# Optimization experiments

Hardware: AMD Instinct MI355X
Metric: run time of the kernel (lower is better)

## Reference

```python
import jax, jax.numpy as jnp
import numpy as np

EPS = 1e-05
H, N, F = 1024, 16, 4096  # hidden_dim, state_dim, ffn_dim


def layernorm(x, g, b):
    mu = jnp.mean(x, axis=-1, keepdims=True)
    var = jnp.mean(jnp.square(x - mu), axis=-1, keepdims=True)
    return (x - mu) * jax.lax.rsqrt(var + EPS) * g + b


def setup_inputs() -> dict:
    key = jax.random.key(0)
    ks = jax.random.split(key, 12)
    B, L = 2, 2048
    s = lambda fan_in: 1.0 / np.sqrt(fan_in)
    inp = {
        "x": jax.random.normal(ks[0], (B, L, H), jnp.float32),
        "ln1_g": jnp.ones((H,), jnp.float32),
        "ln1_b": jnp.zeros((H,), jnp.float32),
        "Wd": jax.random.uniform(ks[1], (H, H), jnp.float32, -s(H), s(H)),
        "bd": jnp.zeros((H,), jnp.float32),
        "Wbc": jax.random.uniform(ks[2], (2 * N, H), jnp.float32, -s(H), s(H)),
        "bbc": jnp.zeros((2 * N,), jnp.float32),
        "A_log": jnp.log(jnp.tile(jnp.arange(1, N + 1, dtype=jnp.float32), (H, 1))),
        "D": jnp.ones((H,), jnp.float32),
        "ln2_g": jnp.ones((H,), jnp.float32),
        "ln2_b": jnp.zeros((H,), jnp.float32),
        "W1": jax.random.uniform(ks[3], (F, H), jnp.float32, -s(H), s(H)),
        "b1": jnp.zeros((F,), jnp.float32),
        "W2": jax.random.uniform(ks[4], (H, F), jnp.float32, -s(F), s(F)),
        "b2": jnp.zeros((H,), jnp.float32),
    }
    return inp


def _selective_ssm(xn, delta, Bm, Cm, A, D):
    # xn: (B,L,H)  delta: (B,L,H)  Bm,Cm: (B,L,N)  A: (H,N)  D: (H,)
    Bsz = xn.shape[0]
    # time-major for scan
    xs = (jnp.moveaxis(delta, 1, 0), jnp.moveaxis(Bm, 1, 0),
          jnp.moveaxis(Cm, 1, 0), jnp.moveaxis(xn, 1, 0))

    def step(h, t):
        d_t, b_t, c_t, x_t = t  # (B,H), (B,N), (B,N), (B,H)
        dA = jnp.exp(d_t[:, :, None] * A)                      # (B,H,N)
        dBx = d_t[:, :, None] * b_t[:, None, :] * x_t[:, :, None]
        h = dA * h + dBx                                       # (B,H,N)
        y = jnp.einsum('bhn,bn->bh', h, c_t)                   # (B,H)
        return h, y

    h0 = jnp.zeros((Bsz, H, N), xn.dtype)
    _, ys = jax.lax.scan(step, h0, xs)
    y = jnp.moveaxis(ys, 0, 1)  # (B,L,H)
    return y + D * xn


def reference(x, ln1_g, ln1_b, Wd, bd, Wbc, bbc, A_log, D,
              ln2_g, ln2_b, W1, b1, W2, b2):
    # --- SSMLayer: pre-norm selective SSM + residual ---
    xn = layernorm(x, ln1_g, ln1_b)
    delta = jax.nn.softplus(xn @ Wd.T + bd)      # (B,L,H)
    bc = xn @ Wbc.T + bbc                        # (B,L,2N)
    Bm, Cm = bc[..., :N], bc[..., N:]
    A = -jnp.exp(A_log)                          # (H,N), negative real
    ssm_out = x + _selective_ssm(xn, delta, Bm, Cm, A, D)
    # --- MambaBlock: norm -> FFN -> residual with ssm_out ---
    normed = layernorm(ssm_out, ln2_g, ln2_b)
    hff = jax.nn.gelu(normed @ W1.T + b1, approximate=False)
    ffn_out = hff @ W2.T + b2
    return ffn_out + ssm_out
```

## Files before the change

### kernel.cpp

```cpp
#include <hip/hip_runtime.h>
#include <cstdint>
#include <cstddef>

typedef unsigned short USHORT;
typedef __bf16 bf16x8 __attribute__((ext_vector_type(8)));
typedef float f32x4 __attribute__((ext_vector_type(4)));

__device__ __forceinline__ float b2f(USHORT u) {
    union { unsigned int i; float f; } v; v.i = ((unsigned int)u) << 16; return v.f;
}
__device__ __forceinline__ USHORT f2bf(float f) {
    union { float f; unsigned int i; } v; v.f = f;
    unsigned int u = v.i;
    unsigned int r = (u + 0x7FFFu + ((u >> 16) & 1u)) >> 16;
    return (USHORT)r;
}
__device__ __forceinline__ float fexp2(float x) { return __builtin_amdgcn_exp2f(x); }

__device__ __forceinline__ void gload_lds16(const void* g, void* l) {
    __builtin_amdgcn_global_load_lds(
        (const __attribute__((address_space(1))) void*)(uintptr_t)g,
        (__attribute__((address_space(3))) void*)(uint32_t)(uintptr_t)l,
        16, 0, 0);
}

__global__ __launch_bounds__(256)
void f2b_all(const float* __restrict__ Wd, const float* __restrict__ W1,
             const float* __restrict__ W2, const float* __restrict__ Wbc,
             USHORT* __restrict__ WdB, USHORT* __restrict__ W1B,
             USHORT* __restrict__ W2B, USHORT* __restrict__ WbcB)
{
    const size_t u = (size_t)blockIdx.x * 256 + threadIdx.x;
    const float* src; USHORT* dst; size_t base;
    if (u < 262144)       { src = Wd;  dst = WdB;  base = 0; }
    else if (u < 1310720) { src = W1;  dst = W1B;  base = 262144; }
    else if (u < 2359296) { src = W2;  dst = W2B;  base = 1310720; }
    else                  { src = Wbc; dst = WbcB; base = 2359296; }
    const size_t i = (u - base) * 4;
    float4 v = *(const float4*)(src + i);
    ushort4 o;
    o.x = f2bf(v.x); o.y = f2bf(v.y); o.z = f2bf(v.z); o.w = f2bf(v.w);
    *(ushort4*)(dst + i) = o;
}

__global__ __launch_bounds__(256)
void ln_kernel(const float* __restrict__ inp, const float* __restrict__ g,
               const float* __restrict__ bsh, USHORT* __restrict__ out)
{
    const int tid = threadIdx.x;
    const int lane = tid & 63;
    const size_t row = (size_t)blockIdx.x * 4 + (tid >> 6);
    const float4* ip = (const float4*)inp + row * 256;
    float4 v[4];
    float s = 0.f, sq = 0.f;
    #pragma unroll
    for (int q = 0; q < 4; q++) {
        v[q] = ip[lane + 64 * q];
        s  += v[q].x + v[q].y + v[q].z + v[q].w;
        sq += v[q].x*v[q].x + v[q].y*v[q].y + v[q].z*v[q].z + v[q].w*v[q].w;
    }
    #pragma unroll
    for (int off = 32; off; off >>= 1) { s += __shfl_xor(s, off); sq += __shfl_xor(sq, off); }
    const float mu = s * (1.0f / 1024.0f);
    const float var = sq * (1.0f / 1024.0f) - mu * mu;
    const float rs = rsqrtf(var + 1e-5f);
    ushort4* op = (ushort4*)out + row * 256;
    #pragma unroll
    for (int q = 0; q < 4; q++) {
        float4 gv = ((const float4*)g)[lane + 64 * q];
        float4 bv = ((const float4*)bsh)[lane + 64 * q];
        ushort4 o;
        o.x = f2bf((v[q].x - mu) * rs * gv.x + bv.x);
        o.y = f2bf((v[q].y - mu) * rs * gv.y + bv.y);
        o.z = f2bf((v[q].z - mu) * rs * gv.z + bv.z);
        o.w = f2bf((v[q].w - mu) * rs * gv.w + bv.w);
        op[lane + 64 * q] = o;
    }
}

template<int EPI>
__global__ __launch_bounds__(256)
void gemm_bt(const USHORT* __restrict__ A, const USHORT* __restrict__ B,
             const float* __restrict__ bias, void* __restrict__ outp,
             void* __restrict__ outp2, int M, int N, int K, int lda, int ldb)
{
    __shared__ __align__(16) unsigned char smem[32768];
    USHORT* As = (USHORT*)smem;
    USHORT* Bs = (USHORT*)(smem + 8192);
    const int tid = threadIdx.x;
    const int lane = tid & 63;
    const int w = tid >> 6;
    const int wr = w >> 1, wc = w & 1;

    const int nx = gridDim.x, ny = gridDim.y;
    const int pid = blockIdx.y * nx + blockIdx.x;
    const int npg = 8 * nx;
    const int gid = pid / npg;
    const int first = gid * 8;
    const int rem = ny - first;
    const int gsz = (rem < 8) ? rem : 8;
    const int py = first + (pid % npg) % gsz;
    const int px = (pid % npg) / gsz;
    const int tm = py * 128;
    const int tn = px * 128;

    f32x4 acc[4][4];
    #pragma unroll
    for (int i = 0; i < 4; i++)
        #pragma unroll
        for (int j = 0; j < 4; j++) acc[i][j] = (f32x4){0.f, 0.f, 0.f, 0.f};

    const int srow = tid >> 2;
    const int scol = (tid & 3) * 8;
    const USHORT* gA0 = A + (size_t)(tm + srow) * lda + scol;
    const USHORT* gA1 = A + (size_t)(tm + 64 + srow) * lda + scol;
    const USHORT* gB0 = B + (size_t)(tn + srow) * ldb + scol;
    const USHORT* gB1 = B + (size_t)(tn + 64 + srow) * ldb + scol;
    USHORT* lA0 = As + w * 512;
    USHORT* lA1 = As + 2048 + w * 512;
    USHORT* lB0 = Bs + w * 512;
    USHORT* lB1 = Bs + 2048 + w * 512;

    const int fr = lane & 15;
    const int fko = (lane >> 4) * 8;
    const int quad = lane >> 4;

    for (int k0 = 0; k0 < K; k0 += 64) {
        gload_lds16(gA0 + k0, lA0);
        gload_lds16(gA1 + k0, lA1);
        gload_lds16(gB0 + k0, lB0);
        gload_lds16(gB1 + k0, lB1);
        gload_lds16(gA0 + k0 + 32, lA0 + 8192);
        gload_lds16(gA1 + k0 + 32, lA1 + 8192);
        gload_lds16(gB0 + k0 + 32, lB0 + 8192);
        gload_lds16(gB1 + k0 + 32, lB1 + 8192);
        __syncthreads();
        #pragma unroll
        for (int h = 0; h < 2; h++) {
            const USHORT* Ah = As + h * 8192;
            const USHORT* Bh = Bs + h * 8192;
            bf16x8 af[4], bfr[4];
            #pragma unroll
            for (int i = 0; i < 4; i++) {
                af[i]  = *(const bf16x8*)(Ah + (wr * 64 + i * 16 + fr) * 32 + fko);
                bfr[i] = *(const bf16x8*)(Bh + (wc * 64 + i * 16 + fr) * 32 + fko);
            }
            #pragma unroll
            for (int i = 0; i < 4; i++)
                #pragma unroll
                for (int j = 0; j < 4; j++)
                    acc[i][j] = __builtin_amdgcn_mfma_f32_16x16x32_bf16(af[i], bfr[j], acc[i][j], 0, 0, 0);
        }
        __syncthreads();
    }

    float* eW = (float*)(smem + (size_t)w * 4352);
    const int rr = lane >> 5;
    const int cc = lane & 31;
    const int gcolb = tn + wc * 64;
    float2 bvv = *(const float2*)&bias[gcolb + cc * 2];

    #pragma unroll
    for (int i = 0; i < 4; i++) {
        #pragma unroll
        for (int j = 0; j < 4; j++)
            #pragma unroll
            for (int r = 0; r < 4; r++)
                eW[(quad * 4 + r) * 68 + j * 16 + fr] = acc[i][j][r];
        __syncthreads();
        const int grow0 = tm + wr * 64 + i * 16;
        #pragma unroll
        for (int rp = 0; rp < 8; rp++) {
            const int row = rp * 2 + rr;
            const float2 v = *(const float2*)&eW[row * 68 + cc * 2];
            const size_t gidx = (size_t)(grow0 + row) * N + gcolb + cc * 2;
            if constexpr (EPI == 2) {
                const float z0 = v.x + bvv.x, z1 = v.y + bvv.y;
                const float o0 = (z0 > 20.f) ? z0 : 0.69314718f * __log2f(1.f + fexp2(z0 * 1.44269504f));
                const float o1 = (z1 > 20.f) ? z1 : 0.69314718f * __log2f(1.f + fexp2(z1 * 1.44269504f));
                *(float2*)((float*)outp + gidx) = make_float2(o0, o1);
            }
        }
        __syncthreads();
    }
    (void)outp2; (void)M;
}

template<int EPI>
__global__ __launch_bounds__(512)
void gemm256(const USHORT* __restrict__ A, const USHORT* __restrict__ B,
             const float* __restrict__ bias, void* __restrict__ outp,
             void* __restrict__ outp2, int M, int N, int K, int lda, int ldb)
{
    __shared__ __align__(16) unsigned char smem[131072];
    const int tid = threadIdx.x;
    const int lane = tid & 63;
    const int w = tid >> 6;
    const int wr = w >> 2;
    const int wc = w & 3;

    const int gx = gridDim.x;
    const int pid = blockIdx.y * gx + blockIdx.x;
    const int nwg = gx * gridDim.y;
    const int cpx = nwg >> 3;
    const int s = (pid & 7) * cpx + (pid >> 3);
    const int c4 = s >> 4;
    const int w4 = s & 15;
    const int py = ((c4 >> 2) << 2) + (w4 >> 2);
    const int px = ((c4 & 3) << 2) + (w4 & 3);
    const int tm = py * 256;
    const int tn = px * 256;

    USHORT* po = nullptr;
    if constexpr (EPI == 3) {
        const int z = blockIdx.z;
        A += (size_t)z * K;
        B += (size_t)z * K;
        po = ((z < 2) ? (USHORT*)outp : (USHORT*)outp2) + (size_t)(z & 1) * ((size_t)M * N);
    }

    const int sr = tid >> 2;
    const int su = (tid & 3) ^ ((tid >> 3) & 3);
    const USHORT* gA0 = A + (size_t)(tm + sr) * lda + su * 8;
    const USHORT* gA1 = A + (size_t)(tm + 128 + sr) * lda + su * 8;
    const USHORT* gB0 = B + (size_t)(tn + sr) * ldb + su * 8;
    const USHORT* gB1 = B + (size_t)(tn + 128 + sr) * ldb + su * 8;

    const int fr = lane & 15;
    const int quad = lane >> 4;
    const int uR = quad ^ ((fr >> 1) & 3);
    const int loff = fr * 32 + uR * 8;

    f32x4 acc[8][4];
    #pragma unroll
    for (int i = 0; i < 8; i++)
        #pragma unroll
        for (int j = 0; j < 4; j++) acc[i][j] = (f32x4){0.f, 0.f, 0.f, 0.f};

    const int NT = K >> 5;

    auto stage = [&](int t) {
        unsigned char* sb = smem + (size_t)(t & 3) * 32768;
        const size_t koff = (size_t)t * 32;
        gload_lds16(gA0 + koff, sb + w * 1024);
        gload_lds16(gA1 + koff, sb + 8192 + w * 1024);
        gload_lds16(gB0 + koff, sb + 16384 + w * 1024);
        gload_lds16(gB1 + koff, sb + 24576 + w * 1024);
    };

    stage(0);
    stage(1);

    for (int t = 0; t < NT; ++t) {
        if (t + 1 < NT) asm volatile("s_waitcnt vmcnt(4)" ::: "memory");
        else            asm volatile("s_waitcnt vmcnt(0)" ::: "memory");
        __builtin_amdgcn_s_barrier();
        if (t + 2 < NT) stage(t + 2);

        const USHORT* sA = (const USHORT*)(smem + (size_t)(t & 3) * 32768);
        const USHORT* sB = sA + 8192;
        bf16x8 a[4], b[4];
        #pragma unroll
        for (int j = 0; j < 4; j++)
            b[j] = *(const bf16x8*)(sB + (wc * 64 + j * 16) * 32 + loff);
        #pragma unroll
        for (int i = 0; i < 4; i++)
            a[i] = *(const bf16x8*)(sA + (wr * 128 + i * 16) * 32 + loff);
        __builtin_amdgcn_s_setprio(1);
        #pragma unroll
        for (int i = 0; i < 4; i++)
            #pragma unroll
            for (int j = 0; j < 4; j++)
                acc[i][j] = __builtin_amdgcn_mfma_f32_16x16x32_bf16(a[i], b[j], acc[i][j], 0, 0, 0);
        __builtin_amdgcn_s_setprio(0);
        #pragma unroll
        for (int i = 0; i < 4; i++)
            a[i] = *(const bf16x8*)(sA + (wr * 128 + 64 + i * 16) * 32 + loff);
        __builtin_amdgcn_s_setprio(1);
        #pragma unroll
        for (int i = 0; i < 4; i++)
            #pragma unroll
            for (int j = 0; j < 4; j++)
                acc[4 + i][j] = __builtin_amdgcn_mfma_f32_16x16x32_bf16(a[i], b[j], acc[4 + i][j], 0, 0, 0);
        __builtin_amdgcn_s_setprio(0);
    }

    float* eW = (float*)(smem + (size_t)w * 4352);
    const int erow = lane >> 2;
    const int ecq = lane & 3;
    const int gcolb = tn + wc * 64 + ecq * 16;
    float bb[16];
    if constexpr (EPI == 1) {
        #pragma unroll
        for (int q = 0; q < 4; q++) {
            float4 bv = *(const float4*)&bias[gcolb + q * 4];
            bb[q*4+0] = bv.x; bb[q*4+1] = bv.y; bb[q*4+2] = bv.z; bb[q*4+3] = bv.w;
        }
    }
    #pragma unroll
    for (int i = 0; i < 8; i++) {
        #pragma unroll
        for (int j = 0; j < 4; j++)
            #pragma unroll
            for (int r = 0; r < 4; r++)
                eW[(quad * 4 + r) * 68 + j * 16 + fr] = acc[i][j][r];
        float v[16];
        #pragma unroll
        for (int q = 0; q < 4; q++) {
            float4 t4 = *(const float4*)&eW[erow * 68 + ecq * 16 + q * 4];
            v[q*4+0] = t4.x; v[q*4+1] = t4.y; v[q*4+2] = t4.z; v[q*4+3] = t4.w;
        }
        const int grow = tm + wr * 128 + i * 16 + erow;
        uint32_t pk[8];
        if constexpr (EPI == 1) {
            #pragma unroll
            for (int q = 0; q < 8; q++) {
                const float z0 = v[2*q]   + bb[2*q];
                const float z1 = v[2*q+1] + bb[2*q+1];
                const float u0 = z0 * (0.7978845608f + 0.035677408f * z0 * z0);
                const float u1 = z1 * (0.7978845608f + 0.035677408f * z1 * z1);
                const float s0 = __builtin_amdgcn_rcpf(1.f + fexp2(2.885390082f * u0));
                const float s1 = __builtin_amdgcn_rcpf(1.f + fexp2(2.885390082f * u1));
                const float g0 = z0 * (1.f - s0), g1 = z1 * (1.f - s1);
                pk[q] = (uint32_t)f2bf(g0) | ((uint32_t)f2bf(g1) << 16);
            }
            USHORT* op = (USHORT*)outp + (size_t)grow * N + gcolb;
            *(uint4*)op = make_uint4(pk[0], pk[1], pk[2], pk[3]);
            *(uint4*)(op + 8) = make_uint4(pk[4], pk[5], pk[6], pk[7]);
        } else {
            #pragma unroll
            for (int q = 0; q < 8; q++)
                pk[q] = (uint32_t)f2bf(v[2*q]) | ((uint32_t)f2bf(v[2*q+1]) << 16);
            USHORT* op = po + (size_t)grow * N + gcolb;
            *(uint4*)op = make_uint4(pk[0], pk[1], pk[2], pk[3]);
            *(uint4*)(op + 8) = make_uint4(pk[4], pk[5], pk[6], pk[7]);
        }
    }
}

template<int EPI>
__global__ __launch_bounds__(512)
void gemm_tlp(const USHORT* __restrict__ A, const USHORT* __restrict__ B,
              const float* __restrict__ bias, void* __restrict__ outp,
              void* __restrict__ outp2, int M, int N, int K, int lda, int ldb)
{
    __shared__ __align__(16) unsigned char smem[73728];
    const int tid = threadIdx.x;
    const int lane = tid & 63;
    const int w = tid >> 6;
    const int wr = w >> 2;
    const int wc = w & 3;

    const int gx = gridDim.x;
    const int pid = blockIdx.y * gx + blockIdx.x;
    const int nwg = gx * gridDim.y;
    const int cpx = nwg >> 3;
    const int sw = (pid & 7) * cpx + (pid >> 3);
    const int tm = (sw >> 2) * 128;
    const int tn = (sw & 3) * 256;

    USHORT* po = nullptr;
    if constexpr (EPI == 3) {
        const int z = blockIdx.z;
        A += (size_t)z * K;
        B += (size_t)z * K;
        po = ((z < 2) ? (USHORT*)outp : (USHORT*)outp2) + (size_t)(z & 1) * ((size_t)M * N);
    }

    const int srow = tid >> 2;
    const int su = (tid & 3) ^ ((tid >> 3) & 3);
    const USHORT* gA  = A + (size_t)(tm + srow) * lda + su * 8;
    const USHORT* gB0 = B + (size_t)(tn + srow) * ldb + su * 8;
    const USHORT* gB1 = B + (size_t)(tn + 128 + srow) * ldb + su * 8;

    const int fr = lane & 15;
    const int quad = lane >> 4;
    const int uR = quad ^ ((fr >> 1) & 3);
    const int loff = fr * 32 + uR * 8;

    f32x4 acc[4][4];
    #pragma unroll
    for (int i = 0; i < 4; i++)
        #pragma unroll
        for (int j = 0; j < 4; j++) acc[i][j] = (f32x4){0.f, 0.f, 0.f, 0.f};

    const int NT = K >> 5;

    auto stage = [&](int t) {
        unsigned char* sb = smem + (size_t)(t % 3) * 24576;
        const size_t ko = (size_t)t * 32;
        gload_lds16(gA  + ko, sb +         w * 1024);
        gload_lds16(gB0 + ko, sb +  8192 + w * 1024);
        gload_lds16(gB1 + ko, sb + 16384 + w * 1024);
    };

    stage(0);
    stage(1);

    for (int t = 0; t < NT; ++t) {
        if (t + 2 < NT) { stage(t + 2); asm volatile("s_waitcnt vmcnt(6)" ::: "memory"); }
        else if (t + 1 < NT) asm volatile("s_waitcnt vmcnt(3)" ::: "memory");
        else                 asm volatile("s_waitcnt vmcnt(0)" ::: "memory");
        __builtin_amdgcn_s_barrier();

        const USHORT* sA = (const USHORT*)(smem + (size_t)(t % 3) * 24576);
        const USHORT* sB = sA + 4096;
        bf16x8 a[4], b[4];
        #pragma unroll
        for (int j = 0; j < 4; j++)
            b[j] = *(const bf16x8*)(sB + (wc * 64 + j * 16) * 32 + loff);
        #pragma unroll
        for (int i = 0; i < 4; i++)
            a[i] = *(const bf16x8*)(sA + (wr * 64 + i * 16) * 32 + loff);
        __builtin_amdgcn_s_setprio(1);
        #pragma unroll
        for (int i = 0; i < 4; i++)
            #pragma unroll
            for (int j = 0; j < 4; j++)
                acc[i][j] = __builtin_amdgcn_mfma_f32_16x16x32_bf16(a[i], b[j], acc[i][j], 0, 0, 0);
        __builtin_amdgcn_s_setprio(0);
        __builtin_amdgcn_s_barrier();
    }

    __syncthreads();
    float* eW = (float*)(smem + (size_t)w * 4352);
    const int erow = lane >> 2;
    const int ecq = lane & 3;
    const int gcolb = tn + wc * 64 + ecq * 16;
    float bb[16];
    if constexpr (EPI == 1) {
        #pragma unroll
        for (int q = 0; q < 4; q++) {
            float4 bv = *(const float4*)&bias[gcolb + q * 4];
            bb[q*4+0] = bv.x; bb[q*4+1] = bv.y; bb[q*4+2] = bv.z; bb[q*4+3] = bv.w;
        }
    }
    #pragma unroll
    for (int i = 0; i < 4; i++) {
        #pragma unroll
        for (int j = 0; j < 4; j++)
            #pragma unroll
            for (int r = 0; r < 4; r++)
                eW[(quad * 4 + r) * 68 + j * 16 + fr] = acc[i][j][r];
        float v[16];
        #pragma unroll
        for (int q = 0; q < 4; q++) {
            float4 t4 = *(const float4*)&eW[erow * 68 + ecq * 16 + q * 4];
            v[q*4+0] = t4.x; v[q*4+1] = t4.y; v[q*4+2] = t4.z; v[q*4+3] = t4.w;
        }
        const int grow = tm + wr * 64 + i * 16 + erow;
        uint32_t pk[8];
        if constexpr (EPI == 1) {
            #pragma unroll
            for (int q = 0; q < 8; q++) {
                const float z0 = v[2*q]   + bb[2*q];
                const float z1 = v[2*q+1] + bb[2*q+1];
                const float u0 = z0 * (0.7978845608f + 0.035677408f * z0 * z0);
                const float u1 = z1 * (0.7978845608f + 0.035677408f * z1 * z1);
                const float s0 = __builtin_amdgcn_rcpf(1.f + fexp2(2.885390082f * u0));
                const float s1 = __builtin_amdgcn_rcpf(1.f + fexp2(2.885390082f * u1));
                const float g0 = z0 * (1.f - s0), g1 = z1 * (1.f - s1);
                pk[q] = (uint32_t)f2bf(g0) | ((uint32_t)f2bf(g1) << 16);
            }
            USHORT* op = (USHORT*)outp + (size_t)grow * N + gcolb;
            *(uint4*)op = make_uint4(pk[0], pk[1], pk[2], pk[3]);
            *(uint4*)(op + 8) = make_uint4(pk[4], pk[5], pk[6], pk[7]);
        } else {
            #pragma unroll
            for (int q = 0; q < 8; q++)
                pk[q] = (uint32_t)f2bf(v[2*q]) | ((uint32_t)f2bf(v[2*q+1]) << 16);
            USHORT* op = po + (size_t)grow * N + gcolb;
            *(uint4*)op = make_uint4(pk[0], pk[1], pk[2], pk[3]);
            *(uint4*)(op + 8) = make_uint4(pk[4], pk[5], pk[6], pk[7]);
        }
    }
    (void)bias;
}

__global__ __launch_bounds__(256)
void ffn2_reduce(const USHORT* __restrict__ p, const float* __restrict__ bias,
                 const float* __restrict__ extra, float* __restrict__ out)
{
    const size_t PS = (size_t)4096 * 1024;
    const size_t i = ((size_t)blockIdx.x * 256 + threadIdx.x) * 4;
    ushort4 a = *(const ushort4*)(p + i);
    ushort4 b = *(const ushort4*)(p + PS + i);
    float4 bv = *(const float4*)(bias + (i & 1023));
    float4 ev = *(const float4*)(extra + i);
    float4 o;
    o.x = b2f(a.x) + b2f(b.x) + bv.x + ev.x;
    o.y = b2f(a.y) + b2f(b.y) + bv.y + ev.y;
    o.z = b2f(a.z) + b2f(b.z) + bv.z + ev.z;
    o.w = b2f(a.w) + b2f(b.w) + bv.w + ev.w;
    *(float4*)(out + i) = o;
}

__global__ __launch_bounds__(256)
void bc_mfma(const USHORT* __restrict__ xn, const USHORT* __restrict__ WbcB,
             const float* __restrict__ bbc, float* __restrict__ bc)
{
    __shared__ __align__(16) USHORT Bs[2][32 * 32];
    __shared__ __align__(16) USHORT As[2][16 * 32];
    const int tid = threadIdx.x;
    const int lane = tid & 63;
    const int w = tid >> 6;
    const int tok0 = blockIdx.x * 16;

    const int fr = lane & 15;
    const int fko = (lane >> 4) * 8;
    const int quad = lane >> 4;

    const int srow = lane >> 2;
    const int scol = (lane & 3) * 8;
    const USHORT* gsrc = nullptr;
    USHORT* ld0 = nullptr; USHORT* ld1 = nullptr;
    if (w == 0)      { gsrc = WbcB + (size_t)srow * 1024 + scol;         ld0 = &Bs[0][0];   ld1 = &Bs[1][0]; }
    else if (w == 1) { gsrc = WbcB + (size_t)(16 + srow) * 1024 + scol;  ld0 = &Bs[0][512]; ld1 = &Bs[1][512]; }
    else if (w == 2) { gsrc = xn + (size_t)(tok0 + srow) * 1024 + scol;  ld0 = &As[0][0];   ld1 = &As[1][0]; }

    f32x4 acc[2];
    acc[0] = (f32x4){0.f, 0.f, 0.f, 0.f};
    acc[1] = (f32x4){0.f, 0.f, 0.f, 0.f};

    if (w < 3) gload_lds16(gsrc, ld0);
    for (int t = 0; t < 32; ++t) {
        if (t + 1 < 32) {
            if (w < 3) gload_lds16(gsrc + (t + 1) * 32, ((t + 1) & 1) ? ld1 : ld0);
            asm volatile("s_waitcnt vmcnt(1)" ::: "memory");
        } else {
            asm volatile("s_waitcnt vmcnt(0)" ::: "memory");
        }
        __syncthreads();
        if (w == 0) {
            const USHORT* Ab = &As[t & 1][0];
            const USHORT* Bb = &Bs[t & 1][0];
            bf16x8 af = *(const bf16x8*)(Ab + fr * 32 + fko);
            bf16x8 b0 = *(const bf16x8*)(Bb + fr * 32 + fko);
            bf16x8 b1 = *(const bf16x8*)(Bb + (16 + fr) * 32 + fko);
            acc[0] = __builtin_amdgcn_mfma_f32_16x16x32_bf16(af, b0, acc[0], 0, 0, 0);
            acc[1] = __builtin_amdgcn_mfma_f32_16x16x32_bf16(af, b1, acc[1], 0, 0, 0);
        }
    }

    if (w == 0) {
        #pragma unroll
        for (int j = 0; j < 2; j++) {
            const int col = j * 16 + fr;
            const float bv = bbc[col];
            #pragma unroll
            for (int r = 0; r < 4; r++)
                bc[(size_t)(tok0 + quad * 4 + r) * 32 + col] = acc[j][r] + bv;
        }
    }
}

#define SCAN_P 64
#define SCAN_T 32

__global__ __launch_bounds__(256)
void scan_pass1(const USHORT* __restrict__ xn, const float* __restrict__ delta,
                const float* __restrict__ bc, const float* __restrict__ Alog,
                float* __restrict__ sEnd, float* __restrict__ Ptot)
{
    const int tid = threadIdx.x;
    const int h = blockIdx.x * 256 + tid;
    const int b = blockIdx.y;
    const int p = blockIdx.z;
    const size_t tok0 = (size_t)b * 2048 + p * SCAN_T;

    __shared__ __align__(16) float sBC[SCAN_T][32];
    {
        int t = tid >> 3, q = (tid & 7) * 4;
        *(float4*)&sBC[t][q] = *(const float4*)(bc + (tok0 + t) * 32 + q);
    }

    float en[16], s[16], P[16];
    #pragma unroll
    for (int k = 0; k < 4; k++) {
        float4 a = *(const float4*)(Alog + h * 16 + k * 4);
        en[k*4+0] = -__expf(a.x) * 1.44269504f;
        en[k*4+1] = -__expf(a.y) * 1.44269504f;
        en[k*4+2] = -__expf(a.z) * 1.44269504f;
        en[k*4+3] = -__expf(a.w) * 1.44269504f;
    }
    #pragma unroll
    for (int n = 0; n < 16; n++) { s[n] = 0.f; P[n] = 1.f; }
    __syncthreads();

    const float* dp = delta + tok0 * 1024 + h;
    const USHORT* xp = xn + tok0 * 1024 + h;
    float d_c = dp[0];
    USHORT x_c = xp[0];
    for (int t = 0; t < SCAN_T; ++t) {
        const int tn = (t < SCAN_T - 1) ? t + 1 : t;
        float d_n = dp[(size_t)tn * 1024];
        USHORT x_n = xp[(size_t)tn * 1024];
        const float dx = d_c * b2f(x_c);
        #pragma unroll
        for (int k = 0; k < 4; k++) {
            float4 Bv = *(const float4*)&sBC[t][k*4];
            float bb[4] = { Bv.x, Bv.y, Bv.z, Bv.w };
            #pragma unroll
            for (int j = 0; j < 4; j++) {
                const int n = k*4 + j;
                const float dA = fexp2(d_c * en[n]);
                s[n] = fmaf(dA, s[n], dx * bb[j]);
                P[n] *= dA;
            }
        }
        d_c = d_n; x_c = x_n;
    }

    const size_t off = (size_t)p * 32768 + ((size_t)b * 1024 + h) * 16;
    #pragma unroll
    for (int k = 0; k < 4; k++) {
        *(float4*)(sEnd + off + k*4) = (float4){ s[k*4], s[k*4+1], s[k*4+2], s[k*4+3] };
        *(float4*)(Ptot + off + k*4) = (float4){ P[k*4], P[k*4+1], P[k*4+2], P[k*4+3] };
    }
}

__global__ __launch_bounds__(256)
void scan_mid(const float* __restrict__ sEnd, const float* __restrict__ Ptot,
              float* __restrict__ sIn)
{
    const int L = blockIdx.x * 256 + threadIdx.x;
    float s = 0.f;
    #pragma unroll 8
    for (int p = 0; p < SCAN_P; ++p) {
        const size_t off = (size_t)p * 32768 + L;
        sIn[off] = s;
        s = fmaf(Ptot[off], s, sEnd[off]);
    }
}

__global__ __launch_bounds__(256)
void scan_pass2(const float* __restrict__ x, const USHORT* __restrict__ xn,
                const float* __restrict__ delta, const float* __restrict__ bc,
                const float* __restrict__ Alog, const float* __restrict__ Dp,
                const float* __restrict__ sIn, float* __restrict__ ssm)
{
    const int tid = threadIdx.x;
    const int h = blockIdx.x * 256 + tid;
    const int b = blockIdx.y;
    const int p = blockIdx.z;
    const size_t tok0 = (size_t)b * 2048 + p * SCAN_T;

    __shared__ __align__(16) float sBC[SCAN_T][32];
    {
        int t = tid >> 3, q = (tid & 7) * 4;
        *(float4*)&sBC[t][q] = *(const float4*)(bc + (tok0 + t) * 32 + q);
    }

    float en[16], s[16];
    #pragma unroll
    for (int k = 0; k < 4; k++) {
        float4 a = *(const float4*)(Alog + h * 16 + k * 4);
        en[k*4+0] = -__expf(a.x) * 1.44269504f;
        en[k*4+1] = -__expf(a.y) * 1.44269504f;
        en[k*4+2] = -__expf(a.z) * 1.44269504f;
        en[k*4+3] = -__expf(a.w) * 1.44269504f;
    }
    const size_t off = (size_t)p * 32768 + ((size_t)b * 1024 + h) * 16;
    #pragma unroll
    for (int k = 0; k < 4; k++) {
        float4 v = *(const float4*)(sIn + off + k*4);
        s[k*4] = v.x; s[k*4+1] = v.y; s[k*4+2] = v.z; s[k*4+3] = v.w;
    }
    const float Dv = Dp[h];
    __syncthreads();

    const float* dp = delta + tok0 * 1024 + h;
    const USHORT* xp = xn + tok0 * 1024 + h;
    const float* xrp = x + tok0 * 1024 + h;
    float* op = ssm + tok0 * 1024 + h;

    float d_c = dp[0];
    USHORT x_c = xp[0];
    float xr_c = xrp[0];
    for (int t = 0; t < SCAN_T; ++t) {
        const int tn = (t < SCAN_T - 1) ? t + 1 : t;
        float d_n = dp[(size_t)tn * 1024];
        USHORT x_n = xp[(size_t)tn * 1024];
        float xr_n = xrp[(size_t)tn * 1024];
        const float xv = b2f(x_c);
        const float dx = d_c * xv;
        float y = 0.f;
        #pragma unroll
        for (int k = 0; k < 4; k++) {
            float4 Bv = *(const float4*)&sBC[t][k*4];
            float4 Cv = *(const float4*)&sBC[t][16 + k*4];
            float bb[4] = { Bv.x, Bv.y, Bv.z, Bv.w };
            float cc[4] = { Cv.x, Cv.y, Cv.z, Cv.w };
            #pragma unroll
            for (int j = 0; j < 4; j++) {
                const int n = k*4 + j;
                const float dA = fexp2(d_c * en[n]);
                s[n] = fmaf(dA, s[n], dx * bb[j]);
                y = fmaf(cc[j], s[n], y);
            }
        }
        op[(size_t)t * 1024] = xr_c + y + Dv * xv;
        d_c = d_n; x_c = x_n; xr_c = xr_n;
    }
}

extern "C" void kernel_launch(void* const* d_in, const int* in_sizes, int n_in,
                              void* d_out, int out_size, void* d_ws, size_t ws_size,
                              hipStream_t stream)
{
    const float* x    = (const float*)d_in[0];
    const float* ln1g = (const float*)d_in[1];
    const float* ln1b = (const float*)d_in[2];
    const float* Wd   = (const float*)d_in[3];
    const float* bd   = (const float*)d_in[4];
    const float* Wbc  = (const float*)d_in[5];
    const float* bbc  = (const float*)d_in[6];
    const float* Alog = (const float*)d_in[7];
    const float* Dp   = (const float*)d_in[8];
    const float* ln2g = (const float*)d_in[9];
    const float* ln2b = (const float*)d_in[10];
    const float* W1   = (const float*)d_in[11];
    const float* b1   = (const float*)d_in[12];
    const float* W2   = (const float*)d_in[13];
    const float* b2   = (const float*)d_in[14];
    float* out = (float*)d_out;

    char* ws = (char*)d_ws;
    const size_t MB = 1024 * 1024;
    float*  deltaW = (float*)(ws + 0);
    float*  ssmW   = (float*)(ws + 16 * MB);
    USHORT* xnW    = (USHORT*)(ws + 32 * MB);
    USHORT* nrmW   = (USHORT*)(ws + 40 * MB);
    USHORT* hffW   = (USHORT*)(ws + 48 * MB);
    float*  bcW    = (float*)(ws + 80 * MB);
    USHORT* WdB    = (USHORT*)(ws + 81 * MB);
    USHORT* W1B    = (USHORT*)(ws + 83 * MB);
    USHORT* W2B    = (USHORT*)(ws + 91 * MB);
    USHORT* WbcB   = (USHORT*)(ws + 99 * MB);
    float*  sEndW  = (float*)(ws + 48 * MB);
    float*  PtotW  = (float*)(ws + 56 * MB);
    float*  sInW   = (float*)(ws + 64 * MB);
    USHORT* ffn2p  = (USHORT*)(ws + 0);

    f2b_all<<<9248, 256, 0, stream>>>(Wd, W1, W2, Wbc, WdB, W1B, W2B, WbcB);
    ln_kernel<<<1024, 256, 0, stream>>>(x, ln1g, ln1b, xnW);
    gemm_bt<2><<<dim3(8, 32), 256, 0, stream>>>(xnW, WdB, bd, deltaW, nullptr, 4096, 1024, 1024, 1024, 1024);
    bc_mfma<<<256, 256, 0, stream>>>(xnW, WbcB, bbc, bcW);
    scan_pass1<<<dim3(4, 2, SCAN_P), 256, 0, stream>>>(xnW, deltaW, bcW, Alog, sEndW, PtotW);
    scan_mid<<<128, 256, 0, stream>>>(sEndW, PtotW, sInW);
    scan_pass2<<<dim3(4, 2, SCAN_P), 256, 0, stream>>>(x, xnW, deltaW, bcW, Alog, Dp, sInW, ssmW);
    ln_kernel<<<1024, 256, 0, stream>>>(ssmW, ln2g, ln2b, nrmW);
    gemm256<1><<<dim3(16, 16), 512, 0, stream>>>(nrmW, W1B, b1, hffW, nullptr, 4096, 4096, 1024, 1024, 1024);
    gemm_tlp<3><<<dim3(32, 4, 2), 512, 0, stream>>>(hffW, W2B, nullptr, ffn2p, nullptr, 4096, 1024, 2048, 4096, 4096);
    ffn2_reduce<<<4096, 256, 0, stream>>>(ffn2p, b2, ssmW, out);

    (void)in_sizes; (void)n_in; (void)out_size; (void)ws_size;
}
```

Measured before the change: 295.4 us.

## Replace split-K FFN2 GEMM and reduce kernel with single fused-epilogue GEMM

The second FFN GEMM used to be split along K into two halves writing bf16 partials, followed by a separate reduce kernel that added bias and the residual. It is now one full-K GEMM with 128x128 tiles over a 32x8 grid, whose epilogue adds the bias and residual and writes fp32 output directly. This removes the partial-sum round trip through memory and one kernel launch, and avoids rounding the partials to bf16. In exchange each block runs a K loop twice as long with a smaller tile, so there is less data reuse per block.

New measurement: 294.9 us. Within noise of the previous version (-0.2%).

```diff
diff --git a/kernel.cpp b/kernel.cpp
--- a/kernel.cpp
+++ b/kernel.cpp
@@ -338,13 +338,12 @@
     }
 }
 
-template<int EPI>
 __global__ __launch_bounds__(512)
-void gemm_tlp(const USHORT* __restrict__ A, const USHORT* __restrict__ B,
-              const float* __restrict__ bias, void* __restrict__ outp,
-              void* __restrict__ outp2, int M, int N, int K, int lda, int ldb)
-{
-    __shared__ __align__(16) unsigned char smem[73728];
+void gemm_tlpf(const USHORT* __restrict__ A, const USHORT* __restrict__ B,
+               const float* __restrict__ bias, const float* __restrict__ extra,
+               float* __restrict__ outp, int K, int lda, int ldb)
+{
+    __shared__ __align__(16) unsigned char smem[49152];
     const int tid = threadIdx.x;
     const int lane = tid & 63;
     const int w = tid >> 6;
@@ -356,59 +355,49 @@
     const int nwg = gx * gridDim.y;
     const int cpx = nwg >> 3;
     const int sw = (pid & 7) * cpx + (pid >> 3);
-    const int tm = (sw >> 2) * 128;
-    const int tn = (sw & 3) * 256;
-
-    USHORT* po = nullptr;
-    if constexpr (EPI == 3) {
-        const int z = blockIdx.z;
-        A += (size_t)z * K;
-        B += (size_t)z * K;
-        po = ((z < 2) ? (USHORT*)outp : (USHORT*)outp2) + (size_t)(z & 1) * ((size_t)M * N);
-    }
+    const int tm = (sw >> 3) * 128;
+    const int tn = (sw & 7) * 128;
 
     const int srow = tid >> 2;
     const int su = (tid & 3) ^ ((tid >> 3) & 3);
-    const USHORT* gA  = A + (size_t)(tm + srow) * lda + su * 8;
-    const USHORT* gB0 = B + (size_t)(tn + srow) * ldb + su * 8;
-    const USHORT* gB1 = B + (size_t)(tn + 128 + srow) * ldb + su * 8;
+    const USHORT* gA = A + (size_t)(tm + srow) * lda + su * 8;
+    const USHORT* gB = B + (size_t)(tn + srow) * ldb + su * 8;
 
     const int fr = lane & 15;
     const int quad = lane >> 4;
     const int uR = quad ^ ((fr >> 1) & 3);
     const int loff = fr * 32 + uR * 8;
 
-    f32x4 acc[4][4];
+    f32x4 acc[4][2];
     #pragma unroll
     for (int i = 0; i < 4; i++)
         #pragma unroll
-        for (int j = 0; j < 4; j++) acc[i][j] = (f32x4){0.f, 0.f, 0.f, 0.f};
+        for (int j = 0; j < 2; j++) acc[i][j] = (f32x4){0.f, 0.f, 0.f, 0.f};
 
     const int NT = K >> 5;
 
     auto stage = [&](int t) {
-        unsigned char* sb = smem + (size_t)(t % 3) * 24576;
+        unsigned char* sb = smem + (size_t)(t % 3) * 16384;
         const size_t ko = (size_t)t * 32;
-        gload_lds16(gA  + ko, sb +         w * 1024);
-        gload_lds16(gB0 + ko, sb +  8192 + w * 1024);
-        gload_lds16(gB1 + ko, sb + 16384 + w * 1024);
+        gload_lds16(gA + ko, sb +        w * 1024);
+        gload_lds16(gB + ko, sb + 8192 + w * 1024);
     };
 
     stage(0);
     stage(1);
 
     for (int t = 0; t < NT; ++t) {
-        if (t + 2 < NT) { stage(t + 2); asm volatile("s_waitcnt vmcnt(6)" ::: "memory"); }
-        else if (t + 1 < NT) asm volatile("s_waitcnt vmcnt(3)" ::: "memory");
+        if (t + 2 < NT) { stage(t + 2); asm volatile("s_waitcnt vmcnt(4)" ::: "memory"); }
+        else if (t + 1 < NT) asm volatile("s_waitcnt vmcnt(2)" ::: "memory");
         else                 asm volatile("s_waitcnt vmcnt(0)" ::: "memory");
         __builtin_amdgcn_s_barrier();
 
-        const USHORT* sA = (const USHORT*)(smem + (size_t)(t % 3) * 24576);
+        const USHORT* sA = (const USHORT*)(smem + (size_t)(t % 3) * 16384);
         const USHORT* sB = sA + 4096;
-        bf16x8 a[4], b[4];
-        #pragma unroll
-        for (int j = 0; j < 4; j++)
-            b[j] = *(const bf16x8*)(sB + (wc * 64 + j * 16) * 32 + loff);
+        bf16x8 a[4], b[2];
+        #pragma unroll
+        for (int j = 0; j < 2; j++)
+            b[j] = *(const bf16x8*)(sB + (wc * 32 + j * 16) * 32 + loff);
         #pragma unroll
         for (int i = 0; i < 4; i++)
             a[i] = *(const bf16x8*)(sA + (wr * 64 + i * 16) * 32 + loff);
@@ -416,83 +405,48 @@
         #pragma unroll
         for (int i = 0; i < 4; i++)
             #pragma unroll
-            for (int j = 0; j < 4; j++)
+            for (int j = 0; j < 2; j++)
                 acc[i][j] = __builtin_amdgcn_mfma_f32_16x16x32_bf16(a[i], b[j], acc[i][j], 0, 0, 0);
         __builtin_amdgcn_s_setprio(0);
         __builtin_amdgcn_s_barrier();
     }
 
     __syncthreads();
-    float* eW = (float*)(smem + (size_t)w * 4352);
+    float* eW = (float*)(smem + (size_t)w * 2304);
     const int erow = lane >> 2;
     const int ecq = lane & 3;
-    const int gcolb = tn + wc * 64 + ecq * 16;
-    float bb[16];
-    if constexpr (EPI == 1) {
-        #pragma unroll
-        for (int q = 0; q < 4; q++) {
-            float4 bv = *(const float4*)&bias[gcolb + q * 4];
-            bb[q*4+0] = bv.x; bb[q*4+1] = bv.y; bb[q*4+2] = bv.z; bb[q*4+3] = bv.w;
-        }
+    const int gcolb = tn + wc * 32 + ecq * 8;
+    float bb[8];
+    #pragma unroll
+    for (int q = 0; q < 2; q++) {
+        float4 bv = *(const float4*)&bias[gcolb + q * 4];
+        bb[q*4+0] = bv.x; bb[q*4+1] = bv.y; bb[q*4+2] = bv.z; bb[q*4+3] = bv.w;
     }
     #pragma unroll
     for (int i = 0; i < 4; i++) {
         #pragma unroll
-        for (int j = 0; j < 4; j++)
+        for (int j = 0; j < 2; j++)
             #pragma unroll
             for (int r = 0; r < 4; r++)
-                eW[(quad * 4 + r) * 68 + j * 16 + fr] = acc[i][j][r];
-        float v[16];
-        #pragma unroll
-        for (int q = 0; q < 4; q++) {
-            float4 t4 = *(const float4*)&eW[erow * 68 + ecq * 16 + q * 4];
+                eW[(quad * 4 + r) * 36 + j * 16 + fr] = acc[i][j][r];
+        float v[8];
+        #pragma unroll
+        for (int q = 0; q < 2; q++) {
+            float4 t4 = *(const float4*)&eW[erow * 36 + ecq * 8 + q * 4];
             v[q*4+0] = t4.x; v[q*4+1] = t4.y; v[q*4+2] = t4.z; v[q*4+3] = t4.w;
         }
         const int grow = tm + wr * 64 + i * 16 + erow;
-        uint32_t pk[8];
-        if constexpr (EPI == 1) {
-            #pragma unroll
-            for (int q = 0; q < 8; q++) {
-                const float z0 = v[2*q]   + bb[2*q];
-                const float z1 = v[2*q+1] + bb[2*q+1];
-                const float u0 = z0 * (0.7978845608f + 0.035677408f * z0 * z0);
-                const float u1 = z1 * (0.7978845608f + 0.035677408f * z1 * z1);
-                const float s0 = __builtin_amdgcn_rcpf(1.f + fexp2(2.885390082f * u0));
-                const float s1 = __builtin_amdgcn_rcpf(1.f + fexp2(2.885390082f * u1));
-                const float g0 = z0 * (1.f - s0), g1 = z1 * (1.f - s1);
-                pk[q] = (uint32_t)f2bf(g0) | ((uint32_t)f2bf(g1) << 16);
-            }
-            USHORT* op = (USHORT*)outp + (size_t)grow * N + gcolb;
-            *(uint4*)op = make_uint4(pk[0], pk[1], pk[2], pk[3]);
-            *(uint4*)(op + 8) = make_uint4(pk[4], pk[5], pk[6], pk[7]);
-        } else {
-            #pragma unroll
-            for (int q = 0; q < 8; q++)
-                pk[q] = (uint32_t)f2bf(v[2*q]) | ((uint32_t)f2bf(v[2*q+1]) << 16);
-            USHORT* op = po + (size_t)grow * N + gcolb;
-            *(uint4*)op = make_uint4(pk[0], pk[1], pk[2], pk[3]);
-            *(uint4*)(op + 8) = make_uint4(pk[4], pk[5], pk[6], pk[7]);
-        }
-    }
-    (void)bias;
-}
-
-__global__ __launch_bounds__(256)
-void ffn2_reduce(const USHORT* __restrict__ p, const float* __restrict__ bias,
-                 const float* __restrict__ extra, float* __restrict__ out)
-{
-    const size_t PS = (size_t)4096 * 1024;
-    const size_t i = ((size_t)blockIdx.x * 256 + threadIdx.x) * 4;
-    ushort4 a = *(const ushort4*)(p + i);
-    ushort4 b = *(const ushort4*)(p + PS + i);
-    float4 bv = *(const float4*)(bias + (i & 1023));
-    float4 ev = *(const float4*)(extra + i);
-    float4 o;
-    o.x = b2f(a.x) + b2f(b.x) + bv.x + ev.x;
-    o.y = b2f(a.y) + b2f(b.y) + bv.y + ev.y;
-    o.z = b2f(a.z) + b2f(b.z) + bv.z + ev.z;
-    o.w = b2f(a.w) + b2f(b.w) + bv.w + ev.w;
-    *(float4*)(out + i) = o;
+        const size_t gidx = (size_t)grow * 1024 + gcolb;
+        float4 e0 = *(const float4*)(extra + gidx);
+        float4 e1 = *(const float4*)(extra + gidx + 4);
+        float4 o0, o1;
+        o0.x = v[0] + bb[0] + e0.x; o0.y = v[1] + bb[1] + e0.y;
+        o0.z = v[2] + bb[2] + e0.z; o0.w = v[3] + bb[3] + e0.w;
+        o1.x = v[4] + bb[4] + e1.x; o1.y = v[5] + bb[5] + e1.y;
+        o1.z = v[6] + bb[6] + e1.z; o1.w = v[7] + bb[7] + e1.w;
+        *(float4*)(outp + gidx) = o0;
+        *(float4*)(outp + gidx + 4) = o1;
+    }
 }
 
 __global__ __launch_bounds__(256)
@@ -740,7 +694,6 @@
     float*  sEndW  = (float*)(ws + 48 * MB);
     float*  PtotW  = (float*)(ws + 56 * MB);
     float*  sInW   = (float*)(ws + 64 * MB);
-    USHORT* ffn2p  = (USHORT*)(ws + 0);
 
     f2b_all<<<9248, 256, 0, stream>>>(Wd, W1, W2, Wbc, WdB, W1B, W2B, WbcB);
     ln_kernel<<<1024, 256, 0, stream>>>(x, ln1g, ln1b, xnW);
@@ -751,8 +704,7 @@
     scan_pass2<<<dim3(4, 2, SCAN_P), 256, 0, stream>>>(x, xnW, deltaW, bcW, Alog, Dp, sInW, ssmW);
     ln_kernel<<<1024, 256, 0, stream>>>(ssmW, ln2g, ln2b, nrmW);
     gemm256<1><<<dim3(16, 16), 512, 0, stream>>>(nrmW, W1B, b1, hffW, nullptr, 4096, 4096, 1024, 1024, 1024);
-    gemm_tlp<3><<<dim3(32, 4, 2), 512, 0, stream>>>(hffW, W2B, nullptr, ffn2p, nullptr, 4096, 1024, 2048, 4096, 4096);
-    ffn2_reduce<<<4096, 256, 0, stream>>>(ffn2p, b2, ssmW, out);
+    gemm_tlpf<<<dim3(32, 8), 512, 0, stream>>>(hffW, W2B, b2, ssmW, out, 4096, 4096, 4096);
 
     (void)in_sizes; (void)n_in; (void)out_size; (void)ws_size;
 }
```
